# Performance work log

Measured on AMD Instinct MI355X. Metric: run time of the kernel, lower is better.

Reference implementation:

```python
import jax, jax.numpy as jnp
import numpy as np

HEADS = 8

def _conv(x, w, b, stride, pad):
    # x: [B,C,H,W], w: [O,I,kh,kw] (torch OIHW layout)
    y = jax.lax.conv_general_dilated(x, w, (stride, stride), ((pad, pad), (pad, pad)),
                                     dimension_numbers=('NCHW', 'OIHW', 'NCHW'))
    return y + b[None, :, None, None]

def _maxpool2x2(x):
    # returns pooled values and one-hot argmax per 2x2 window (torch first-max tie-break)
    b, c, H, W = x.shape
    win = x.reshape(b, c, H // 2, 2, W // 2, 2).transpose(0, 1, 2, 4, 3, 5).reshape(b, c, H // 2, W // 2, 4)
    am = jnp.argmax(win, axis=-1)
    oh = jax.nn.one_hot(am, 4, dtype=x.dtype)
    pooled = jnp.sum(win * oh, axis=-1)
    return pooled, oh

def _maxunpool2x2(y, oh):
    b, c, h2, w2 = y.shape
    out = y[..., None] * oh  # [b,c,h2,w2,4]
    out = out.reshape(b, c, h2, w2, 2, 2).transpose(0, 1, 2, 4, 3, 5).reshape(b, c, h2 * 2, w2 * 2)
    return out

def _mha2d(x, wq, wk, wv, wo):
    # x: [b,c,h,w]; wq/wk/wv/wo stored as [in,out] so y = x @ W
    b, c, h, w = x.shape
    hw = h * w
    dk = wq.shape[1]
    dh = dk // HEADS
    xt = x.reshape(b, c, hw).transpose(0, 2, 1)  # [b,hw,c]
    def split(y):  # torch: view(b,hw,dh,heads).permute(0,3,1,2)
        return y.reshape(b, hw, dh, HEADS).transpose(0, 3, 1, 2)  # [b,heads,hw,dh]
    q = split(xt @ wq)
    k = split(xt @ wk)
    v = split(xt @ wv)
    scale = jnp.sqrt(jnp.asarray(dh, x.dtype))
    attn = jax.nn.softmax(jnp.einsum('bhqd,bhkd->bhqk', q, k) / scale, axis=-1)
    o = jnp.einsum('bhqk,bhkd->bhqd', attn, v)
    o = o.transpose(0, 2, 3, 1).reshape(b, hw, dk)  # [b,hw,dh,heads] -> merge
    o = o @ wo
    return o.transpose(0, 2, 1).reshape(b, dk, h, w)

def setup_inputs() -> dict:
    key = jax.random.key(0)
    ks = jax.random.split(key, 10)
    B, C, H, W = 16, 256, 64, 64
    s = 0.05
    return {
        'x': jax.random.normal(ks[0], (B, C, H, W), jnp.float32),
        'conv_w': jax.random.normal(ks[1], (C, C, 3, 3), jnp.float32) * s,
        'conv_b': jax.random.normal(ks[2], (C,), jnp.float32) * s,
        'fr_w': jax.random.normal(ks[3], (C, C, 1, 1), jnp.float32) * s,
        'fr_b': jax.random.normal(ks[4], (C,), jnp.float32) * s,
        'wq': jax.random.normal(ks[5], (C, C), jnp.float32) * s,
        'wk': jax.random.normal(ks[6], (C, C), jnp.float32) * s,
        'wv': jax.random.normal(ks[7], (C, C), jnp.float32) * s,
        'wo': jax.random.normal(ks[8], (C, C), jnp.float32) * s,
        'gamma': jax.random.normal(ks[9], (1,), jnp.float32) * 0.1,
    }

def reference(x, conv_w, conv_b, fr_w, fr_b, wq, wk, wv, wo, gamma):
    _x = _conv(x, fr_w, fr_b, 1, 0)          # 1x1 feature reduction
    _x, oh = _maxpool2x2(_x)                 # MaxPool2d(2, return_indices=True)
    _x = _mha2d(_x, wq, wk, wv, wo)          # attention over pooled grid
    _x = _maxunpool2x2(_x, oh)               # MaxUnpool2d(2)
    return _x * jnp.tanh(gamma[0]) + _conv(x, conv_w, conv_b, 1, 1)
```

## Files before the change

### kernel.cpp

```cpp
#include <hip/hip_runtime.h>
#include <hip/hip_bf16.h>
#include <math.h>

#define B 16
#define C 256
#define H 64
#define W 64
#define H2 32
#define W2 32
#define HW2 1024
#define HEADS 8
#define DH 32

typedef unsigned short ushort_t;
using short8 = __attribute__((ext_vector_type(8))) short;
using u16x8  = __attribute__((ext_vector_type(8))) unsigned short;
using f32x4  = __attribute__((ext_vector_type(4))) float;

__device__ inline ushort_t f2bf(float f) {
    __hip_bfloat16 hb = __float2bfloat16(f);
    return *(ushort_t*)&hb;
}
__device__ inline float bf2f(ushort_t u) {
    return __uint_as_float(((unsigned)u) << 16);
}

__device__ __forceinline__ void cp16(const ushort_t* g, ushort_t* l) {
    __builtin_amdgcn_global_load_lds(
        (const __attribute__((address_space(1))) void*)g,
        (__attribute__((address_space(3))) void*)l, 16, 0, 0);
}

#define RSCALE 0.17677669529663687f

__global__ __launch_bounds__(256) void k_prep_wT(const float* __restrict__ cw,
                                                 ushort_t* __restrict__ wbfT) {
    int i = threadIdx.x, o = blockIdx.x;
    const float* src = cw + ((size_t)o * C + i) * 9;
#pragma unroll
    for (int kk = 0; kk < 9; kk++)
        wbfT[((size_t)kk * C + o) * C + i] = f2bf(src[kk]);
}

__global__ __launch_bounds__(256) void k_prep_wx(
    const float* __restrict__ wq, const float* __restrict__ wk,
    const float* __restrict__ wv, const float* __restrict__ wo,
    const float* __restrict__ frw, ushort_t* __restrict__ wqkvT,
    ushort_t* __restrict__ woT, ushort_t* __restrict__ wfr) {
    int op = blockIdx.x, mat = blockIdx.y, t = threadIdx.x;
    if (mat < 3) {
        const float* w = (mat == 0) ? wq : (mat == 1) ? wk : wv;
        int hh = op >> 5, d = op & 31, col = d * 8 + hh;
        wqkvT[(size_t)mat * 65536 + op * 256 + t] = f2bf(w[t * 256 + col]);
    } else if (mat == 3) {
        int hh = t >> 5, d = t & 31, ic = d * 8 + hh;
        woT[op * 256 + t] = f2bf(wo[ic * 256 + op]);
    } else {
        wfr[op * 256 + t] = f2bf(frw[op * 256 + t]);
    }
}

__global__ __launch_bounds__(256) void k_prep_xn(const float* __restrict__ x,
                                                 ushort_t* __restrict__ xn) {
    __shared__ ushort_t ldsT[64 * 258];
    int t = threadIdx.x;
    int hp = blockIdx.x, b = blockIdx.y;
    ushort_t* dst = xn + ((size_t)(b * 66 + hp)) * 66 * 256;

    if (hp == 0 || hp == 65) {
        u16x8 z = (u16x8){0, 0, 0, 0, 0, 0, 0, 0};
        for (int i = t; i < 2112; i += 256) *(u16x8*)(dst + i * 8) = z;
        return;
    }
    const float* xb = x + ((size_t)b * 256) * 4096 + (size_t)(hp - 1) * 64;
    {
        int cq = t >> 6, w = t & 63;
#pragma unroll 8
        for (int it = 0; it < 64; ++it) {
            int c = it * 4 + cq;
            float v = xb[(size_t)c * 4096 + w];
            ldsT[w * 258 + c] = f2bf(v);
        }
    }
    __syncthreads();
    {
        u16x8 z = (u16x8){0, 0, 0, 0, 0, 0, 0, 0};
        if (t < 32) *(u16x8*)(dst + t * 8) = z;
        else if (t < 64) *(u16x8*)(dst + 65 * 256 + (t - 32) * 8) = z;
    }
    {
        int half = t >> 7, cl = t & 127;
#pragma unroll 4
        for (int it = 0; it < 32; ++it) {
            int w = it * 2 + half;
            unsigned v = *(const unsigned*)&ldsT[w * 258 + cl * 2];
            *(unsigned*)(dst + (size_t)(w + 1) * 256 + cl * 2) = v;
        }
    }
}

__global__ __launch_bounds__(256) void k_conv1pool_mfma(
    const ushort_t* __restrict__ xn, const ushort_t* __restrict__ wfr,
    const float* __restrict__ frb, ushort_t* __restrict__ Pbf,
    unsigned char* __restrict__ idx) {
    __shared__ __align__(16) ushort_t sh[32768];
    ushort_t* Als = sh;
    ushort_t* Bls = sh + 8192;
    int t = threadIdx.x;
    int wg = blockIdx.x;
    int mt = (wg & 7) * 64 + (wg >> 3);
    int b = mt >> 5;
    int h0 = (mt * 2) & 63;

    int r = t >> 2, p = t & 3;
    int kswz = (p ^ ((r >> 1) & 3)) * 8;
    const ushort_t* aB0 = xn + ((size_t)((b * 66 + h0 + 1) * 66 + (r + 1))) * 256 + kswz;
    const ushort_t* aB1 = xn + ((size_t)((b * 66 + h0 + 2) * 66 + (r + 1))) * 256 + kswz;
    const ushort_t* bB = wfr + (size_t)r * 256 + kswz;

    f32x4 acc[4][8];
#pragma unroll
    for (int mf = 0; mf < 4; mf++)
#pragma unroll
        for (int nf = 0; nf < 8; nf++) acc[mf][nf] = (f32x4){0.f, 0.f, 0.f, 0.f};

    cp16(aB0, &Als[t * 8]);
    cp16(aB1, &Als[2048 + t * 8]);
    cp16(bB, &Bls[t * 8]);
    cp16(bB + 64 * 256, &Bls[2048 + t * 8]);
    cp16(bB + 128 * 256, &Bls[4096 + t * 8]);
    cp16(bB + 192 * 256, &Bls[6144 + t * 8]);
    __syncthreads();

    int l = t & 63, wid = t >> 6, wm = wid >> 1, wn = wid & 1;
    int arow = wm * 64 + (l & 15);
    int brow = wn * 128 + (l & 15);
    int pslot = ((l >> 4) ^ ((l >> 1) & 3)) * 8;

    for (int s = 0; s < 8; s++) {
        int cur = s & 1;
        if (s < 7) {
            int off = (s + 1) * 32;
            int nb = cur ^ 1;
            cp16(aB0 + off, &Als[nb * 4096 + t * 8]);
            cp16(aB1 + off, &Als[nb * 4096 + 2048 + t * 8]);
            cp16(bB + off, &Bls[nb * 8192 + t * 8]);
            cp16(bB + 64 * 256 + off, &Bls[nb * 8192 + 2048 + t * 8]);
            cp16(bB + 128 * 256 + off, &Bls[nb * 8192 + 4096 + t * 8]);
            cp16(bB + 192 * 256 + off, &Bls[nb * 8192 + 6144 + t * 8]);
        }
        short8 af[4], bf[8];
#pragma unroll
        for (int mf = 0; mf < 4; mf++)
            af[mf] = *(const short8*)&Als[cur * 4096 + (arow + mf * 16) * 32 + pslot];
#pragma unroll
        for (int nf = 0; nf < 8; nf++)
            bf[nf] = *(const short8*)&Bls[cur * 8192 + (brow + nf * 16) * 32 + pslot];
#pragma unroll
        for (int mf = 0; mf < 4; mf++)
#pragma unroll
            for (int nf = 0; nf < 8; nf++)
                acc[mf][nf] = __builtin_amdgcn_mfma_f32_16x16x32_bf16(
                    af[mf], bf[nf], acc[mf][nf], 0, 0, 0);
        __syncthreads();
    }

#pragma unroll
    for (int nf = 0; nf < 8; nf++) {
        int o = wn * 128 + nf * 16 + (l & 15);
        float bias = frb[o];
#pragma unroll
        for (int mf = 0; mf < 4; mf++) {
            int rbase = wm * 64 + mf * 16 + ((l >> 4) << 2);
            f32x4 a = acc[mf][nf];
#pragma unroll
            for (int jj = 0; jj < 4; jj++)
                sh[(rbase + jj) * 256 + o] = f2bf(a[jj] + bias);
        }
    }
    __syncthreads();

    {
        int h2 = mt & 31;
        size_t rowb = (size_t)(b << 10) + h2 * 32;
        int o0 = (t & 31) * 8;
#pragma unroll
        for (int pp = 0; pp < 4; pp++) {
            int w2 = pp * 8 + (t >> 5);
            u16x8 r0 = *(const u16x8*)&sh[(2 * w2) * 256 + o0];
            u16x8 r1 = *(const u16x8*)&sh[(2 * w2 + 1) * 256 + o0];
            u16x8 r2 = *(const u16x8*)&sh[(64 + 2 * w2) * 256 + o0];
            u16x8 r3 = *(const u16x8*)&sh[(64 + 2 * w2 + 1) * 256 + o0];
            u16x8 pv;
            unsigned amlo = 0, amhi = 0;
#pragma unroll
            for (int e = 0; e < 8; e++) {
                float v0 = bf2f(r0[e]), v1 = bf2f(r1[e]);
                float v2 = bf2f(r2[e]), v3 = bf2f(r3[e]);
                float m = v0;
                ushort_t raw = r0[e];
                unsigned am = 0;
                if (v1 > m) { m = v1; raw = r1[e]; am = 1; }
                if (v2 > m) { m = v2; raw = r2[e]; am = 2; }
                if (v3 > m) { m = v3; raw = r3[e]; am = 3; }
                pv[e] = raw;
                if (e < 4) amlo |= am << (8 * e);
                else       amhi |= am << (8 * (e - 4));
            }
            size_t po = (rowb + w2) * 256 + o0;
            *(u16x8*)(Pbf + po) = pv;
            *(uint2*)(idx + po) = make_uint2(amlo, amhi);
        }
    }
}

__global__ __launch_bounds__(256) void k_qkv_mfma(
    const ushort_t* __restrict__ A, const ushort_t* __restrict__ Bw,
    ushort_t* __restrict__ qb, ushort_t* __restrict__ kb,
    ushort_t* __restrict__ vtb) {
    __shared__ __align__(16) ushort_t Als[2][4096];
    __shared__ __align__(16) ushort_t Bls[2][4096];
    int t = threadIdx.x;
    int wg = blockIdx.x;
    int linear = (wg & 7) * 96 + (wg >> 3);
    int mt = linear / 6, nt = linear % 6;

    int r = t >> 2, p = t & 3;
    int kswz = (p ^ ((r >> 1) & 3)) * 8;
    const ushort_t* aB0 = A + ((size_t)(mt * 128 + r)) * 256 + kswz;
    const ushort_t* aB1 = aB0 + (size_t)64 * 256;
    const ushort_t* bB0 = Bw + ((size_t)(nt * 128 + r)) * 256 + kswz;
    const ushort_t* bB1 = bB0 + (size_t)64 * 256;

    f32x4 acc[4][4];
#pragma unroll
    for (int mf = 0; mf < 4; mf++)
#pragma unroll
        for (int nf = 0; nf < 4; nf++) acc[mf][nf] = (f32x4){0.f, 0.f, 0.f, 0.f};

    cp16(aB0, &Als[0][t * 8]);
    cp16(aB1, &Als[0][2048 + t * 8]);
    cp16(bB0, &Bls[0][t * 8]);
    cp16(bB1, &Bls[0][2048 + t * 8]);
    __syncthreads();

    int l = t & 63, wid = t >> 6, wm = wid >> 1, wn = wid & 1;
    int arow = wm * 64 + (l & 15);
    int brow = wn * 64 + (l & 15);
    int pslot = ((l >> 4) ^ ((l >> 1) & 3)) * 8;

    for (int s = 0; s < 8; s++) {
        int cur = s & 1;
        if (s < 7) {
            int off = (s + 1) * 32;
            int nb = cur ^ 1;
            cp16(aB0 + off, &Als[nb][t * 8]);
            cp16(aB1 + off, &Als[nb][2048 + t * 8]);
            cp16(bB0 + off, &Bls[nb][t * 8]);
            cp16(bB1 + off, &Bls[nb][2048 + t * 8]);
        }
        short8 af[4], bf[4];
#pragma unroll
        for (int mf = 0; mf < 4; mf++)
            af[mf] = *(const short8*)&Als[cur][(arow + mf * 16) * 32 + pslot];
#pragma unroll
        for (int nf = 0; nf < 4; nf++)
            bf[nf] = *(const short8*)&Bls[cur][(brow + nf * 16) * 32 + pslot];
#pragma unroll
        for (int mf = 0; mf < 4; mf++)
#pragma unroll
            for (int nf = 0; nf < 4; nf++)
                acc[mf][nf] = __builtin_amdgcn_mfma_f32_16x16x32_bf16(
                    af[mf], bf[nf], acc[mf][nf], 0, 0, 0);
        __syncthreads();
    }

    if (nt < 4) {
        ushort_t* dst = (nt < 2) ? qb : kb;
        float sc = (nt < 2) ? RSCALE : 1.0f;
        int ccb = (nt & 1) * 128 + wn * 64;
#pragma unroll
        for (int nf = 0; nf < 4; nf++) {
            int cc = ccb + nf * 16 + (l & 15);
#pragma unroll
            for (int mf = 0; mf < 4; mf++) {
                int m = mt * 128 + wm * 64 + mf * 16 + ((l >> 4) << 2);
                f32x4 a = acc[mf][nf];
#pragma unroll
                for (int jj = 0; jj < 4; jj++)
                    dst[(size_t)(m + jj) * 256 + cc] = f2bf(a[jj] * sc);
            }
        }
    } else {
#pragma unroll
        for (int nf = 0; nf < 4; nf++) {
            int cc = (nt & 1) * 128 + wn * 64 + nf * 16 + (l & 15);
#pragma unroll
            for (int mf = 0; mf < 4; mf++) {
                int m = mt * 128 + wm * 64 + mf * 16 + ((l >> 4) << 2);
                int b = m >> 10, n0 = m & 1023;
                f32x4 a = acc[mf][nf];
                unsigned u0 = ((unsigned)f2bf(a[1]) << 16) | f2bf(a[0]);
                unsigned u1 = ((unsigned)f2bf(a[3]) << 16) | f2bf(a[2]);
                *(uint2*)&vtb[((size_t)(b * 256 + cc)) * 1024 + n0] =
                    make_uint2(u0, u1);
            }
        }
    }
}

__global__ __launch_bounds__(256) void k_attn_mfma(
    const ushort_t* __restrict__ qb, const ushort_t* __restrict__ kb,
    const ushort_t* __restrict__ vtb, ushort_t* __restrict__ aoT) {
    __shared__ __align__(16) ushort_t Klds[2][2048];
    __shared__ __align__(16) ushort_t Vlds[2][2048];
    __shared__ __align__(16) ushort_t Plds[4][2304];
    __shared__ float rs_lds[128];

    int t = threadIdx.x;
    int bid = blockIdx.x;
    int swz = (bid & 7) * 128 + (bid >> 3);
    int bh = swz >> 3, qt = swz & 7;
    int b = bh >> 3, h = bh & 7;
    int w = t >> 6, l = t & 63, g = l >> 4, li = l & 15;

    size_t qrow = (size_t)(b * 1024 + qt * 128 + w * 32 + li);
    short8 qv0 = *(const short8*)(qb + qrow * 256 + h * 32 + g * 8);
    short8 qv1 = *(const short8*)(qb + (qrow + 16) * 256 + h * 32 + g * 8);

    int sr = t >> 2, sp = t & 3;
    const ushort_t* kg =
        kb + ((size_t)(b * 1024 + sr)) * 256 + h * 32 + ((sp ^ ((sr >> 1) & 3)) * 8);
    int vd = t >> 3, vs = t & 7;
    const ushort_t* vg =
        vtb + ((size_t)(b * 256 + h * 32 + vd)) * 1024 + ((vs ^ (vd & 7)) * 8);

    f32x4 oacc[2][2];
    f32x4 rsv[2];
#pragma unroll
    for (int qf = 0; qf < 2; qf++) {
        rsv[qf] = (f32x4){0.f, 0.f, 0.f, 0.f};
#pragma unroll
        for (int df = 0; df < 2; df++) oacc[qf][df] = (f32x4){0.f, 0.f, 0.f, 0.f};
    }

    cp16(kg, &Klds[0][t * 8]);
    cp16(vg, &Vlds[0][t * 8]);
    __syncthreads();

    ushort_t* Pw = &Plds[w][0];

    for (int c = 0; c < 16; c++) {
        int cur = c & 1;
        if (c < 15) {
            cp16(kg + (size_t)(c + 1) * 64 * 256, &Klds[cur ^ 1][t * 8]);
            cp16(vg + (c + 1) * 64, &Vlds[cur ^ 1][t * 8]);
        }
        short8 ak[4];
#pragma unroll
        for (int kf = 0; kf < 4; kf++)
            ak[kf] = *(const short8*)&Klds[cur][(16 * kf + li) * 32 +
                                               ((g ^ ((l >> 1) & 3)) * 8)];
#pragma unroll
        for (int qf = 0; qf < 2; qf++) {
            short8 qv = qf ? qv1 : qv0;
#pragma unroll
            for (int kf = 0; kf < 4; kf++) {
                f32x4 st = __builtin_amdgcn_mfma_f32_16x16x32_bf16(
                    ak[kf], qv, (f32x4){0.f, 0.f, 0.f, 0.f}, 0, 0, 0);
                float p0 = __expf(st[0]), p1 = __expf(st[1]);
                float p2 = __expf(st[2]), p3 = __expf(st[3]);
                rsv[qf][0] += p0; rsv[qf][1] += p1;
                rsv[qf][2] += p2; rsv[qf][3] += p3;
                unsigned u0, u1;
                asm("v_cvt_pk_bf16_f32 %0, %1, %2" : "=v"(u0) : "v"(p0), "v"(p1));
                asm("v_cvt_pk_bf16_f32 %0, %1, %2" : "=v"(u1) : "v"(p2), "v"(p3));
                *(uint2*)&Pw[(16 * qf + li) * 72 + 16 * kf + 4 * g] =
                    make_uint2(u0, u1);
            }
        }
#pragma unroll
        for (int win = 0; win < 2; win++) {
            short8 pa[2], bv[2];
#pragma unroll
            for (int qf = 0; qf < 2; qf++)
                pa[qf] = *(const short8*)&Pw[(16 * qf + li) * 72 + win * 32 + 8 * g];
#pragma unroll
            for (int df = 0; df < 2; df++)
                bv[df] = *(const short8*)&Vlds[cur][(16 * df + li) * 64 +
                                                    (((win * 4 + g) ^ (l & 7)) * 8)];
#pragma unroll
            for (int qf = 0; qf < 2; qf++)
#pragma unroll
                for (int df = 0; df < 2; df++)
                    oacc[qf][df] = __builtin_amdgcn_mfma_f32_16x16x32_bf16(
                        pa[qf], bv[df], oacc[qf][df], 0, 0, 0);
        }
        __syncthreads();
    }

#pragma unroll
    for (int qf = 0; qf < 2; qf++) {
        float rs = (rsv[qf][0] + rsv[qf][1]) + (rsv[qf][2] + rsv[qf][3]);
        rs += __shfl_xor(rs, 16);
        rs += __shfl_xor(rs, 32);
        if (l < 16) rs_lds[w * 32 + 16 * qf + li] = rs;
    }
    __syncthreads();

#pragma unroll
    for (int qf = 0; qf < 2; qf++) {
        float4 rs4 = *(const float4*)&rs_lds[w * 32 + 16 * qf + 4 * g];
        float inv[4] = {1.f / rs4.x, 1.f / rs4.y, 1.f / rs4.z, 1.f / rs4.w};
#pragma unroll
        for (int df = 0; df < 2; df++) {
            f32x4 a = oacc[qf][df];
#pragma unroll
            for (int r2 = 0; r2 < 4; r2++) {
                size_t row = (size_t)(b * 1024 + qt * 128 + w * 32 + 16 * qf +
                                      4 * g + r2);
                aoT[row * 256 + h * 32 + 16 * df + li] = f2bf(a[r2] * inv[r2]);
            }
        }
    }
}

__global__ __launch_bounds__(256) void k_oproj_mfma(
    const ushort_t* __restrict__ A, const ushort_t* __restrict__ Bw,
    float* __restrict__ y2) {
    __shared__ __align__(16) ushort_t Als[2][4096];
    __shared__ __align__(16) ushort_t Bls[2][4096];
    int t = threadIdx.x;
    int wg = blockIdx.x;
    int linear = (wg & 7) * 32 + (wg >> 3);
    int nt = linear & 1, mt = linear >> 1;

    int r = t >> 2, p = t & 3;
    int kswz = (p ^ ((r >> 1) & 3)) * 8;
    const ushort_t* aB0 = A + ((size_t)(mt * 128 + r)) * 256 + kswz;
    const ushort_t* aB1 = aB0 + (size_t)64 * 256;
    const ushort_t* bB0 = Bw + ((size_t)(nt * 128 + r)) * 256 + kswz;
    const ushort_t* bB1 = bB0 + (size_t)64 * 256;

    f32x4 acc[4][4];
#pragma unroll
    for (int mf = 0; mf < 4; mf++)
#pragma unroll
        for (int nf = 0; nf < 4; nf++) acc[mf][nf] = (f32x4){0.f, 0.f, 0.f, 0.f};

    cp16(aB0, &Als[0][t * 8]);
    cp16(aB1, &Als[0][2048 + t * 8]);
    cp16(bB0, &Bls[0][t * 8]);
    cp16(bB1, &Bls[0][2048 + t * 8]);
    __syncthreads();

    int l = t & 63, wid = t >> 6, wm = wid >> 1, wn = wid & 1;
    int arow = wm * 64 + (l & 15);
    int brow = wn * 64 + (l & 15);
    int pslot = ((l >> 4) ^ ((l >> 1) & 3)) * 8;

    for (int s = 0; s < 8; s++) {
        int cur = s & 1;
        if (s < 7) {
            int off = (s + 1) * 32;
            int nb = cur ^ 1;
            cp16(aB0 + off, &Als[nb][t * 8]);
            cp16(aB1 + off, &Als[nb][2048 + t * 8]);
            cp16(bB0 + off, &Bls[nb][t * 8]);
            cp16(bB1 + off, &Bls[nb][2048 + t * 8]);
        }
        short8 af[4], bf[4];
#pragma unroll
        for (int mf = 0; mf < 4; mf++)
            af[mf] = *(const short8*)&Als[cur][(arow + mf * 16) * 32 + pslot];
#pragma unroll
        for (int nf = 0; nf < 4; nf++)
            bf[nf] = *(const short8*)&Bls[cur][(brow + nf * 16) * 32 + pslot];
#pragma unroll
        for (int mf = 0; mf < 4; mf++)
#pragma unroll
            for (int nf = 0; nf < 4; nf++)
                acc[mf][nf] = __builtin_amdgcn_mfma_f32_16x16x32_bf16(
                    af[mf], bf[nf], acc[mf][nf], 0, 0, 0);
        __syncthreads();
    }

#pragma unroll
    for (int nf = 0; nf < 4; nf++) {
        int cc = nt * 128 + wn * 64 + nf * 16 + (l & 15);
#pragma unroll
        for (int mf = 0; mf < 4; mf++) {
            int m = mt * 128 + wm * 64 + mf * 16 + ((l >> 4) << 2);
            f32x4 a = acc[mf][nf];
#pragma unroll
            for (int jj = 0; jj < 4; jj++)
                y2[(size_t)(m + jj) * 256 + cc] = a[jj];
        }
    }
}

__global__ __launch_bounds__(256) void k_conv3_mfma(
    const ushort_t* __restrict__ xn, const ushort_t* __restrict__ wbfT,
    const float* __restrict__ cb, const float* __restrict__ y2,
    const unsigned char* __restrict__ idx, const float* __restrict__ gamma,
    float* __restrict__ out) {
    __shared__ __align__(16) ushort_t Als[2][8192];
    __shared__ __align__(16) ushort_t Bls[2][8192];
    int t = threadIdx.x;
    int wg = blockIdx.x;
    int swz = (wg & 7) * 128 + (wg >> 3);
    int nt = swz & 1, mt = swz >> 1;

    int sr = t >> 3, sslot = t & 7;
    int kel = (sslot ^ (sr & 7)) * 8;
    const ushort_t* aB[4];
    const ushort_t* bB[4];
#pragma unroll
    for (int i = 0; i < 4; i++) {
        int row = i * 32 + sr;
        int m = mt * 128 + row;
        int b0 = m >> 12, h0 = (m >> 6) & 63, w0 = m & 63;
        aB[i] = xn + ((size_t)((b0 * 66 + h0) * 66 + w0)) * 256 + kel;
        bB[i] = wbfT + ((size_t)(nt * 128 + row)) * 256 + kel;
    }

    f32x4 acc[4][4];
#pragma unroll
    for (int mf = 0; mf < 4; mf++)
#pragma unroll
        for (int nf = 0; nf < 4; nf++) acc[mf][nf] = (f32x4){0.f, 0.f, 0.f, 0.f};

    auto STAGE = [&](int s, int tb) {
        int khkw = s >> 2, it = s & 3;
        int kh = khkw / 3, kw = khkw - kh * 3;
        size_t offA = (size_t)(kh * 66 + kw) * 256 + it * 64;
        size_t offB = (size_t)khkw * 65536 + it * 64;
#pragma unroll
        for (int i = 0; i < 4; i++) {
            cp16(aB[i] + offA, &Als[tb][(i * 256 + t) * 8]);
            cp16(bB[i] + offB, &Bls[tb][(i * 256 + t) * 8]);
        }
    };

    int l = t & 63, wid = t >> 6, wm = wid >> 1, wn = wid & 1;
    int g = l >> 4, lr = l & 15, l7 = l & 7;

    STAGE(0, 0);
    __syncthreads();

    for (int s = 0; s < 36; s++) {
        int cur = s & 1;
        if (s < 35) STAGE(s + 1, cur ^ 1);
        short8 af[2][4], bf[2][4];
#pragma unroll
        for (int kk = 0; kk < 2; kk++) {
            int sl = ((kk * 4 + g) ^ l7) * 8;
#pragma unroll
            for (int mf = 0; mf < 4; mf++)
                af[kk][mf] =
                    *(const short8*)&Als[cur][(wm * 64 + mf * 16 + lr) * 64 + sl];
#pragma unroll
            for (int nf = 0; nf < 4; nf++)
                bf[kk][nf] =
                    *(const short8*)&Bls[cur][(wn * 64 + nf * 16 + lr) * 64 + sl];
        }
#pragma unroll
        for (int kk = 0; kk < 2; kk++)
#pragma unroll
            for (int mf = 0; mf < 4; mf++)
#pragma unroll
                for (int nf = 0; nf < 4; nf++)
                    acc[mf][nf] = __builtin_amdgcn_mfma_f32_16x16x32_bf16(
                        af[kk][mf], bf[kk][nf], acc[mf][nf], 0, 0, 0);
        __syncthreads();
    }

    float tg = tanhf(gamma[0]);
    int mbase = mt * 128 + wm * 64 + ((l >> 4) << 2);
    int obase = nt * 128 + wn * 64 + (l & 15);
#pragma unroll
    for (int nf = 0; nf < 4; nf++) {
        int o = obase + nf * 16;
        float bias = cb[o];
#pragma unroll
        for (int mf = 0; mf < 4; mf++) {
            int m = mbase + mf * 16;
            int b = m >> 12, h = (m >> 6) & 63, w0 = m & 63;
            const unsigned char* idr = idx + ((size_t)(b << 10)) * 256;
            const float* y2r = y2 + ((size_t)(b << 10)) * 256;
            f32x4 a = acc[mf][nf];
            float v4[4];
#pragma unroll
            for (int jj = 0; jj < 4; jj++) {
                int wj = w0 + jj;
                int n2 = ((h >> 1) << 5) + (wj >> 1);
                int j2 = ((h & 1) << 1) + (wj & 1);
                float val = a[jj] + bias;
                if (idr[(size_t)n2 * 256 + o] == (unsigned char)j2)
                    val += tg * y2r[(size_t)n2 * 256 + o];
                v4[jj] = val;
            }
            *(float4*)(out + (((size_t)(b * C + o) * H + h) << 6) + w0) =
                make_float4(v4[0], v4[1], v4[2], v4[3]);
        }
    }
}

extern "C" void kernel_launch(void* const* d_in, const int* in_sizes, int n_in,
                              void* d_out, int out_size, void* d_ws, size_t ws_size,
                              hipStream_t stream) {
    const float* x      = (const float*)d_in[0];
    const float* conv_w = (const float*)d_in[1];
    const float* conv_b = (const float*)d_in[2];
    const float* fr_w   = (const float*)d_in[3];
    const float* fr_b   = (const float*)d_in[4];
    const float* wq     = (const float*)d_in[5];
    const float* wk     = (const float*)d_in[6];
    const float* wv     = (const float*)d_in[7];
    const float* wo     = (const float*)d_in[8];
    const float* gamma  = (const float*)d_in[9];
    float* out = (float*)d_out;
    char* ws = (char*)d_ws;

    ushort_t* wbfT  = (ushort_t*)(ws + 0);
    ushort_t* wfrbf = (ushort_t*)(ws + 1179648);
    ushort_t* wqkvT = (ushort_t*)(ws + 1310720);
    ushort_t* woT   = (ushort_t*)(ws + 1703936);
    ushort_t* xn    = (ushort_t*)(ws + 2097152);
    ushort_t* Pbf   = (ushort_t*)(ws + 37781504);
    unsigned char* idx = (unsigned char*)(ws + 46170112);
    ushort_t* qb    = (ushort_t*)(ws + 50364416);
    ushort_t* kb    = (ushort_t*)(ws + 58753024);
    ushort_t* vtb   = (ushort_t*)(ws + 67141632);
    ushort_t* aoT   = (ushort_t*)(ws + 75530240);
    float* y2       = (float*)(ws + 50364416);

    k_prep_wT<<<dim3(C), dim3(256), 0, stream>>>(conv_w, wbfT);
    k_prep_wx<<<dim3(256, 5), dim3(256), 0, stream>>>(wq, wk, wv, wo, fr_w,
                                                      wqkvT, woT, wfrbf);
    k_prep_xn<<<dim3(66, B), dim3(256), 0, stream>>>(x, xn);
    k_conv1pool_mfma<<<dim3(512), dim3(256), 0, stream>>>(xn, wfrbf, fr_b, Pbf, idx);
    k_qkv_mfma<<<dim3(768), dim3(256), 0, stream>>>(Pbf, wqkvT, qb, kb, vtb);
    k_attn_mfma<<<dim3(1024), dim3(256), 0, stream>>>(qb, kb, vtb, aoT);
    k_oproj_mfma<<<dim3(256), dim3(256), 0, stream>>>(aoT, woT, y2);
    k_conv3_mfma<<<dim3(1024), dim3(256), 0, stream>>>(xn, wbfT, conv_b, y2, idx,
                                                       gamma, out);
    (void)in_sizes; (void)n_in; (void)out_size; (void)ws_size;
}
```

Baseline: 244.4 us.

## Restructure 3x3 conv GEMM into 256x256 tiles with 8-wave ping-pong pipeline

The implicit-GEMM 3x3 convolution now uses 256x256 output tiles per workgroup with 512 threads, and 128KB of dynamic LDS split into double-buffered A/B halves. Each K step is divided into four MFMA quadrants. Global-to-LDS copies for the next stages are interleaved between them, using explicit barriers, sched_barrier and s_setprio to overlap loads with matrix math. This doubles data reuse per tile and hides memory latency, at the cost of fewer workgroups (256), heavy LDS use limiting occupancy, and fragile hand-tuned synchronisation.

```diff
diff --git a/kernel.cpp b/kernel.cpp
--- a/kernel.cpp
+++ b/kernel.cpp
@@ -499,91 +499,182 @@
     }
 }
 
-__global__ __launch_bounds__(256) void k_conv3_mfma(
+__global__ __launch_bounds__(512) void k_conv3_mfma(
     const ushort_t* __restrict__ xn, const ushort_t* __restrict__ wbfT,
     const float* __restrict__ cb, const float* __restrict__ y2,
     const unsigned char* __restrict__ idx, const float* __restrict__ gamma,
     float* __restrict__ out) {
-    __shared__ __align__(16) ushort_t Als[2][8192];
-    __shared__ __align__(16) ushort_t Bls[2][8192];
+    extern __shared__ __align__(16) ushort_t lds[];
+    ushort_t* AL = lds;
+    ushort_t* BL = lds + 32768;
     int t = threadIdx.x;
-    int wg = blockIdx.x;
-    int swz = (wg & 7) * 128 + (wg >> 3);
-    int nt = swz & 1, mt = swz >> 1;
-
-    int sr = t >> 3, sslot = t & 7;
-    int kel = (sslot ^ (sr & 7)) * 8;
-    const ushort_t* aB[4];
-    const ushort_t* bB[4];
-#pragma unroll
-    for (int i = 0; i < 4; i++) {
-        int row = i * 32 + sr;
-        int m = mt * 128 + row;
-        int b0 = m >> 12, h0 = (m >> 6) & 63, w0 = m & 63;
-        aB[i] = xn + ((size_t)((b0 * 66 + h0) * 66 + w0)) * 256 + kel;
-        bB[i] = wbfT + ((size_t)(nt * 128 + row)) * 256 + kel;
-    }
-
-    f32x4 acc[4][4];
-#pragma unroll
-    for (int mf = 0; mf < 4; mf++)
+    int mt = blockIdx.x;
+
+    int srow = t >> 3, sslot = t & 7;
+    int kel = (sslot ^ (srow & 7)) * 8;
+    const ushort_t* aP[2][2];
+    const ushort_t* bP[2][2];
+#pragma unroll
+    for (int hf = 0; hf < 2; hf++)
+#pragma unroll
+        for (int j = 0; j < 2; j++) {
+            int row = hf * 128 + j * 64 + srow;
+            int m = mt * 256 + row;
+            int b0 = m >> 12, h0 = (m >> 6) & 63, w0 = m & 63;
+            aP[hf][j] = xn + ((size_t)((b0 * 66 + h0) * 66 + w0)) * 256 + kel;
+            bP[hf][j] = wbfT + (size_t)row * 256 + kel;
+        }
+
+    auto offA = [](int kt) -> int {
+        int khkw = kt >> 2, it = kt & 3;
+        int kh = khkw / 3, kw = khkw - kh * 3;
+        return (kh * 66 + kw) * 256 + it * 64;
+    };
+    auto offB = [](int kt) -> int {
+        return (kt >> 2) * 65536 + (kt & 3) * 64;
+    };
+    auto STAGE_A = [&](int bb, int hf, int kt) {
+        int o = offA(kt);
+        ushort_t* d = AL + bb * 16384 + hf * 8192 + t * 8;
+        cp16(aP[hf][0] + o, d);
+        cp16(aP[hf][1] + o, d + 4096);
+    };
+    auto STAGE_B = [&](int bb, int hf, int kt) {
+        int o = offB(kt);
+        ushort_t* d = BL + bb * 16384 + hf * 8192 + t * 8;
+        cp16(bP[hf][0] + o, d);
+        cp16(bP[hf][1] + o, d + 4096);
+    };
+
+    f32x4 acc[8][4];
+#pragma unroll
+    for (int mf = 0; mf < 8; mf++)
 #pragma unroll
         for (int nf = 0; nf < 4; nf++) acc[mf][nf] = (f32x4){0.f, 0.f, 0.f, 0.f};
 
-    auto STAGE = [&](int s, int tb) {
-        int khkw = s >> 2, it = s & 3;
-        int kh = khkw / 3, kw = khkw - kh * 3;
-        size_t offA = (size_t)(kh * 66 + kw) * 256 + it * 64;
-        size_t offB = (size_t)khkw * 65536 + it * 64;
-#pragma unroll
-        for (int i = 0; i < 4; i++) {
-            cp16(aB[i] + offA, &Als[tb][(i * 256 + t) * 8]);
-            cp16(bB[i] + offB, &Bls[tb][(i * 256 + t) * 8]);
-        }
-    };
-
-    int l = t & 63, wid = t >> 6, wm = wid >> 1, wn = wid & 1;
-    int g = l >> 4, lr = l & 15, l7 = l & 7;
-
-    STAGE(0, 0);
-    __syncthreads();
-
-    for (int s = 0; s < 36; s++) {
-        int cur = s & 1;
-        if (s < 35) STAGE(s + 1, cur ^ 1);
-        short8 af[2][4], bf[2][4];
-#pragma unroll
-        for (int kk = 0; kk < 2; kk++) {
-            int sl = ((kk * 4 + g) ^ l7) * 8;
+    STAGE_A(0, 0, 0); STAGE_A(0, 1, 0); STAGE_B(0, 0, 0); STAGE_B(0, 1, 0);
+    STAGE_B(1, 0, 1); STAGE_A(1, 0, 1);
+    asm volatile("s_waitcnt vmcnt(4)" ::: "memory");
+    __builtin_amdgcn_s_barrier();
+    __builtin_amdgcn_sched_barrier(0);
+
+    int l = t & 63, wid = t >> 6, wm = wid >> 2, wn = wid & 3;
+    int lr = l & 15, g = l >> 4, l7 = l & 7;
+    int abase = wm * 8192;
+    int bbase = (wn >> 1) * 8192 + (wn & 1) * 4096;
+
+    for (int kt = 0; kt < 36; kt++) {
+        int bb = kt & 1;
+        const ushort_t* Ab = AL + bb * 16384 + abase;
+        const ushort_t* Bb = BL + bb * 16384 + bbase;
+        short8 afA[4][2], afB[4][2], bf0[2][2], bf1[2][2];
+#pragma unroll
+        for (int mf = 0; mf < 4; mf++)
+#pragma unroll
+            for (int kk = 0; kk < 2; kk++)
+                afA[mf][kk] = *(const short8*)
+                    &Ab[(mf * 16 + lr) * 64 + (((kk * 4 + g) ^ l7) * 8)];
+#pragma unroll
+        for (int nf = 0; nf < 2; nf++)
+#pragma unroll
+            for (int kk = 0; kk < 2; kk++)
+                bf0[nf][kk] = *(const short8*)
+                    &Bb[(nf * 16 + lr) * 64 + (((kk * 4 + g) ^ l7) * 8)];
+        if (kt < 35) STAGE_A(bb ^ 1, 1, kt + 1);
+        asm volatile("" ::: "memory");
+        __builtin_amdgcn_s_barrier();
+        __builtin_amdgcn_sched_barrier(0);
+        __builtin_amdgcn_s_setprio(1);
+#pragma unroll
+        for (int kk = 0; kk < 2; kk++)
 #pragma unroll
             for (int mf = 0; mf < 4; mf++)
-                af[kk][mf] =
-                    *(const short8*)&Als[cur][(wm * 64 + mf * 16 + lr) * 64 + sl];
-#pragma unroll
-            for (int nf = 0; nf < 4; nf++)
-                bf[kk][nf] =
-                    *(const short8*)&Bls[cur][(wn * 64 + nf * 16 + lr) * 64 + sl];
-        }
+#pragma unroll
+                for (int nf = 0; nf < 2; nf++)
+                    acc[mf][nf] = __builtin_amdgcn_mfma_f32_16x16x32_bf16(
+                        afA[mf][kk], bf0[nf][kk], acc[mf][nf], 0, 0, 0);
+        __builtin_amdgcn_s_setprio(0);
+        asm volatile("" ::: "memory");
+        __builtin_amdgcn_s_barrier();
+        __builtin_amdgcn_sched_barrier(0);
+#pragma unroll
+        for (int nf = 0; nf < 2; nf++)
+#pragma unroll
+            for (int kk = 0; kk < 2; kk++)
+                bf1[nf][kk] = *(const short8*)
+                    &Bb[((nf + 2) * 16 + lr) * 64 + (((kk * 4 + g) ^ l7) * 8)];
+        if (kt < 35) STAGE_B(bb ^ 1, 1, kt + 1);
+        asm volatile("" ::: "memory");
+        __builtin_amdgcn_s_barrier();
+        __builtin_amdgcn_sched_barrier(0);
+        __builtin_amdgcn_s_setprio(1);
 #pragma unroll
         for (int kk = 0; kk < 2; kk++)
 #pragma unroll
             for (int mf = 0; mf < 4; mf++)
 #pragma unroll
-                for (int nf = 0; nf < 4; nf++)
-                    acc[mf][nf] = __builtin_amdgcn_mfma_f32_16x16x32_bf16(
-                        af[kk][mf], bf[kk][nf], acc[mf][nf], 0, 0, 0);
-        __syncthreads();
+                for (int nf = 0; nf < 2; nf++)
+                    acc[mf][nf + 2] = __builtin_amdgcn_mfma_f32_16x16x32_bf16(
+                        afA[mf][kk], bf1[nf][kk], acc[mf][nf + 2], 0, 0, 0);
+        __builtin_amdgcn_s_setprio(0);
+        asm volatile("" ::: "memory");
+        __builtin_amdgcn_s_barrier();
+        __builtin_amdgcn_sched_barrier(0);
+#pragma unroll
+        for (int mf = 0; mf < 4; mf++)
+#pragma unroll
+            for (int kk = 0; kk < 2; kk++)
+                afB[mf][kk] = *(const short8*)
+                    &Ab[((mf + 4) * 16 + lr) * 64 + (((kk * 4 + g) ^ l7) * 8)];
+        if (kt < 34) STAGE_B(bb, 0, kt + 2);
+        asm volatile("" ::: "memory");
+        __builtin_amdgcn_s_barrier();
+        __builtin_amdgcn_sched_barrier(0);
+        __builtin_amdgcn_s_setprio(1);
+#pragma unroll
+        for (int kk = 0; kk < 2; kk++)
+#pragma unroll
+            for (int mf = 0; mf < 4; mf++)
+#pragma unroll
+                for (int nf = 0; nf < 2; nf++)
+                    acc[mf + 4][nf] = __builtin_amdgcn_mfma_f32_16x16x32_bf16(
+                        afB[mf][kk], bf0[nf][kk], acc[mf + 4][nf], 0, 0, 0);
+        __builtin_amdgcn_s_setprio(0);
+        asm volatile("" ::: "memory");
+        __builtin_amdgcn_s_barrier();
+        __builtin_amdgcn_sched_barrier(0);
+        if (kt < 34) {
+            STAGE_A(bb, 0, kt + 2);
+            asm volatile("s_waitcnt vmcnt(4)" ::: "memory");
+        } else {
+            asm volatile("s_waitcnt vmcnt(0)" ::: "memory");
+        }
+        __builtin_amdgcn_s_barrier();
+        __builtin_amdgcn_sched_barrier(0);
+        __builtin_amdgcn_s_setprio(1);
+#pragma unroll
+        for (int kk = 0; kk < 2; kk++)
+#pragma unroll
+            for (int mf = 0; mf < 4; mf++)
+#pragma unroll
+                for (int nf = 0; nf < 2; nf++)
+                    acc[mf + 4][nf + 2] = __builtin_amdgcn_mfma_f32_16x16x32_bf16(
+                        afB[mf][kk], bf1[nf][kk], acc[mf + 4][nf + 2], 0, 0, 0);
+        __builtin_amdgcn_s_setprio(0);
+        asm volatile("" ::: "memory");
+        __builtin_amdgcn_s_barrier();
+        __builtin_amdgcn_sched_barrier(0);
     }
 
     float tg = tanhf(gamma[0]);
-    int mbase = mt * 128 + wm * 64 + ((l >> 4) << 2);
-    int obase = nt * 128 + wn * 64 + (l & 15);
+    int mbase = mt * 256 + wm * 128 + (g << 2);
+    int obase = wn * 64 + lr;
 #pragma unroll
     for (int nf = 0; nf < 4; nf++) {
         int o = obase + nf * 16;
         float bias = cb[o];
 #pragma unroll
-        for (int mf = 0; mf < 4; mf++) {
+        for (int mf = 0; mf < 8; mf++) {
             int m = mbase + mf * 16;
             int b = m >> 12, h = (m >> 6) & 63, w0 = m & 63;
             const unsigned char* idr = idx + ((size_t)(b << 10)) * 256;
@@ -643,7 +734,9 @@
     k_qkv_mfma<<<dim3(768), dim3(256), 0, stream>>>(Pbf, wqkvT, qb, kb, vtb);
     k_attn_mfma<<<dim3(1024), dim3(256), 0, stream>>>(qb, kb, vtb, aoT);
     k_oproj_mfma<<<dim3(256), dim3(256), 0, stream>>>(aoT, woT, y2);
-    k_conv3_mfma<<<dim3(1024), dim3(256), 0, stream>>>(xn, wbfT, conv_b, y2, idx,
-                                                       gamma, out);
+    (void)hipFuncSetAttribute(reinterpret_cast<const void*>(k_conv3_mfma),
+                              hipFuncAttributeMaxDynamicSharedMemorySize, 131072);
+    k_conv3_mfma<<<dim3(256), dim3(512), 131072, stream>>>(xn, wbfT, conv_b, y2, idx,
+                                                           gamma, out);
     (void)in_sizes; (void)n_in; (void)out_size; (void)ws_size;
 }
```

Result: faster. 219.6 us (-10.2%).

## Retile 3x3 conv GEMM to 128x256 blocks with 512 threads and K=32 stages

Applied to the files above, without the earlier changes.

The 3x3 convolution implicit GEMM now gives each 512-thread block a 128x256 output tile covering all output channels, where it used to be two 128x128 tiles. This halves the grid and means each input activation tile is loaded once instead of twice. The K step per stage shrinks from 64 to 32, so there are 72 stages, and the LDS swizzle is rewritten for the narrower rows. The trade-off is more barriers per unit of work and lower per-stage MFMA density, in exchange for less redundant global/LDS traffic on A and a smaller LDS footprint.

```diff
diff --git a/kernel.cpp b/kernel.cpp
--- a/kernel.cpp
+++ b/kernel.cpp
@@ -499,30 +499,40 @@
     }
 }
 
-__global__ __launch_bounds__(256) void k_conv3_mfma(
+__global__ __launch_bounds__(512, 4) void k_conv3_mfma(
     const ushort_t* __restrict__ xn, const ushort_t* __restrict__ wbfT,
     const float* __restrict__ cb, const float* __restrict__ y2,
     const unsigned char* __restrict__ idx, const float* __restrict__ gamma,
     float* __restrict__ out) {
-    __shared__ __align__(16) ushort_t Als[2][8192];
-    __shared__ __align__(16) ushort_t Bls[2][8192];
+    __shared__ __align__(16) ushort_t AL[2][4096];
+    __shared__ __align__(16) ushort_t BL[2][8192];
     int t = threadIdx.x;
     int wg = blockIdx.x;
-    int swz = (wg & 7) * 128 + (wg >> 3);
-    int nt = swz & 1, mt = swz >> 1;
-
-    int sr = t >> 3, sslot = t & 7;
-    int kel = (sslot ^ (sr & 7)) * 8;
-    const ushort_t* aB[4];
-    const ushort_t* bB[4];
-#pragma unroll
-    for (int i = 0; i < 4; i++) {
-        int row = i * 32 + sr;
-        int m = mt * 128 + row;
-        int b0 = m >> 12, h0 = (m >> 6) & 63, w0 = m & 63;
-        aB[i] = xn + ((size_t)((b0 * 66 + h0) * 66 + w0)) * 256 + kel;
-        bB[i] = wbfT + ((size_t)(nt * 128 + row)) * 256 + kel;
-    }
+    int mt = (wg & 7) * 64 + (wg >> 3);
+
+    int srow = t >> 2, sslot = t & 3;
+    int kel = (sslot ^ ((srow >> 1) & 3)) * 8;
+    int m0 = mt * 128 + srow;
+    int ab0 = m0 >> 12, ah0 = (m0 >> 6) & 63, aw0 = m0 & 63;
+    const ushort_t* aP = xn + ((size_t)((ab0 * 66 + ah0) * 66 + aw0)) * 256 + kel;
+    const ushort_t* bP0 = wbfT + (size_t)srow * 256 + kel;
+    const ushort_t* bP1 = wbfT + (size_t)(srow + 128) * 256 + kel;
+
+    auto offA = [](int kt) -> int {
+        int it = kt / 9, khkw = kt - it * 9;
+        int kh = khkw / 3, kw = khkw - kh * 3;
+        return (kh * 66 + kw) * 256 + it * 32;
+    };
+    auto offB = [](int kt) -> int {
+        int it = kt / 9, khkw = kt - it * 9;
+        return khkw * 65536 + it * 32;
+    };
+    auto STAGE = [&](int bb, int kt) {
+        cp16(aP + offA(kt), &AL[bb][t * 8]);
+        int ob = offB(kt);
+        cp16(bP0 + ob, &BL[bb][t * 8]);
+        cp16(bP1 + ob, &BL[bb][4096 + t * 8]);
+    };
 
     f32x4 acc[4][4];
 #pragma unroll
@@ -530,54 +540,35 @@
 #pragma unroll
         for (int nf = 0; nf < 4; nf++) acc[mf][nf] = (f32x4){0.f, 0.f, 0.f, 0.f};
 
-    auto STAGE = [&](int s, int tb) {
-        int khkw = s >> 2, it = s & 3;
-        int kh = khkw / 3, kw = khkw - kh * 3;
-        size_t offA = (size_t)(kh * 66 + kw) * 256 + it * 64;
-        size_t offB = (size_t)khkw * 65536 + it * 64;
-#pragma unroll
-        for (int i = 0; i < 4; i++) {
-            cp16(aB[i] + offA, &Als[tb][(i * 256 + t) * 8]);
-            cp16(bB[i] + offB, &Bls[tb][(i * 256 + t) * 8]);
-        }
-    };
-
-    int l = t & 63, wid = t >> 6, wm = wid >> 1, wn = wid & 1;
-    int g = l >> 4, lr = l & 15, l7 = l & 7;
+    int l = t & 63, wid = t >> 6, wm = wid >> 2, wn = wid & 3;
+    int lr = l & 15, g = l >> 4;
+    int fslot = (g ^ ((lr >> 1) & 3)) * 8;
 
     STAGE(0, 0);
     __syncthreads();
 
-    for (int s = 0; s < 36; s++) {
-        int cur = s & 1;
-        if (s < 35) STAGE(s + 1, cur ^ 1);
-        short8 af[2][4], bf[2][4];
-#pragma unroll
-        for (int kk = 0; kk < 2; kk++) {
-            int sl = ((kk * 4 + g) ^ l7) * 8;
-#pragma unroll
-            for (int mf = 0; mf < 4; mf++)
-                af[kk][mf] =
-                    *(const short8*)&Als[cur][(wm * 64 + mf * 16 + lr) * 64 + sl];
+    for (int kt = 0; kt < 72; kt++) {
+        int cur = kt & 1;
+        if (kt < 71) STAGE(cur ^ 1, kt + 1);
+        short8 af[4], bf[4];
+#pragma unroll
+        for (int mf = 0; mf < 4; mf++)
+            af[mf] = *(const short8*)&AL[cur][(wm * 64 + mf * 16 + lr) * 32 + fslot];
+#pragma unroll
+        for (int nf = 0; nf < 4; nf++)
+            bf[nf] = *(const short8*)&BL[cur][(wn * 64 + nf * 16 + lr) * 32 + fslot];
+#pragma unroll
+        for (int mf = 0; mf < 4; mf++)
 #pragma unroll
             for (int nf = 0; nf < 4; nf++)
-                bf[kk][nf] =
-                    *(const short8*)&Bls[cur][(wn * 64 + nf * 16 + lr) * 64 + sl];
-        }
-#pragma unroll
-        for (int kk = 0; kk < 2; kk++)
-#pragma unroll
-            for (int mf = 0; mf < 4; mf++)
-#pragma unroll
-                for (int nf = 0; nf < 4; nf++)
-                    acc[mf][nf] = __builtin_amdgcn_mfma_f32_16x16x32_bf16(
-                        af[kk][mf], bf[kk][nf], acc[mf][nf], 0, 0, 0);
+                acc[mf][nf] = __builtin_amdgcn_mfma_f32_16x16x32_bf16(
+                    af[mf], bf[nf], acc[mf][nf], 0, 0, 0);
         __syncthreads();
     }
 
     float tg = tanhf(gamma[0]);
-    int mbase = mt * 128 + wm * 64 + ((l >> 4) << 2);
-    int obase = nt * 128 + wn * 64 + (l & 15);
+    int mbase = mt * 128 + wm * 64 + (g << 2);
+    int obase = wn * 64 + lr;
 #pragma unroll
     for (int nf = 0; nf < 4; nf++) {
         int o = obase + nf * 16;
@@ -643,7 +634,7 @@
     k_qkv_mfma<<<dim3(768), dim3(256), 0, stream>>>(Pbf, wqkvT, qb, kb, vtb);
     k_attn_mfma<<<dim3(1024), dim3(256), 0, stream>>>(qb, kb, vtb, aoT);
     k_oproj_mfma<<<dim3(256), dim3(256), 0, stream>>>(aoT, woT, y2);
-    k_conv3_mfma<<<dim3(1024), dim3(256), 0, stream>>>(xn, wbfT, conv_b, y2, idx,
-                                                       gamma, out);
+    k_conv3_mfma<<<dim3(512), dim3(512), 0, stream>>>(xn, wbfT, conv_b, y2, idx,
+                                                      gamma, out);
     (void)in_sizes; (void)n_in; (void)out_size; (void)ws_size;
 }
```

Measured after the change: 211.2 us. 1.16x faster.
